# Optimization experiments

Hardware: AMD Instinct MI355X
Metric: run time of the kernel (lower is better)

Reference implementation:

```python
import jax, jax.numpy as jnp
import numpy as np

B, C, T, D = 4, 64, 256, 256   # batch, channel, time, in_feat
H, DK, OUT = 4, 64, 256        # heads, d_k, out_feat
MIN_VALUE = float(np.finfo(np.float32).min)


def _complex_linear(xr, xi, wr, wi, br, bi):
    # ComplexLinear: (fc_r(xr) - fc_i(xi), fc_r(xi) + fc_i(xr))
    out_r = (xr @ wr + br) - (xi @ wi + bi)
    out_i = (xi @ wr + br) + (xr @ wi + bi)
    return out_r, out_i


def setup_inputs() -> dict:
    key = jax.random.key(0)
    ks = jax.random.split(key, 23)
    s = 1.0 / np.sqrt(D)
    inp = {}
    names = ['q_r', 'q_i', 'k_r', 'k_i', 'v_r', 'v_i']
    for i, n in enumerate(names):
        inp[n] = jax.random.normal(ks[i], (B, C, T, D), dtype=jnp.float32)
    inp['mask'] = jnp.ones((B, 1, C), dtype=jnp.int32)
    pi = 6
    for proj in ['q', 'k', 'v', 'o']:
        out_dim = OUT if proj == 'o' else D
        inp[f'w{proj}_r'] = jax.random.normal(ks[pi], (D, out_dim), dtype=jnp.float32) * s; pi += 1
        inp[f'w{proj}_i'] = jax.random.normal(ks[pi], (D, out_dim), dtype=jnp.float32) * s; pi += 1
        inp[f'b{proj}_r'] = jax.random.normal(ks[pi], (out_dim,), dtype=jnp.float32) * 0.01; pi += 1
        inp[f'b{proj}_i'] = jax.random.normal(ks[pi], (out_dim,), dtype=jnp.float32) * 0.01; pi += 1
    return inp


def _split_heads(x):
    # (B, C, T, D) -> (B, H, T, C, DK)  [view + transpose(1,3)]
    return x.reshape(B, C, T, H, DK).transpose(0, 3, 2, 1, 4)


def _attention(q_r, q_i, k_r, k_i, v_r, v_i, mask,
               wq_r, wq_i, bq_r, bq_i, wk_r, wk_i, bk_r, bk_i,
               wv_r, wv_i, bv_r, bv_i, wo_r, wo_i, bo_r, bo_i):
    qr, qi = _complex_linear(q_r, q_i, wq_r, wq_i, bq_r, bq_i)
    kr, ki = _complex_linear(k_r, k_i, wk_r, wk_i, bk_r, bk_i)
    vr, vi = _complex_linear(v_r, v_i, wv_r, wv_i, bv_r, bv_i)
    qr, qi, kr, ki, vr, vi = map(_split_heads, (qr, qi, kr, ki, vr, vi))

    # scores = conj(q) @ k^T  (conjugate_transpose_matmul_conjugate), scaled by 1/sqrt(d_k)
    scale = 1.0 / np.sqrt(DK)
    s_r = (jnp.einsum('bhtcd,bhted->bhtce', qr, kr)
           + jnp.einsum('bhtcd,bhted->bhtce', qi, ki)) * scale
    s_i = (jnp.einsum('bhtcd,bhted->bhtce', qr, ki)
           - jnp.einsum('bhtcd,bhted->bhtce', qi, kr)) * scale

    # amplitude softmax with masking (mask: (B,1,C) -> (B,1,1,1,C), eq(0))
    mask_b = (mask == 0)[:, None, None]  # (B,1,1,1,C)
    amp = jnp.sqrt(s_r * s_r + s_i * s_i)
    amp = jnp.where(mask_b, MIN_VALUE, amp)
    sc = jax.nn.softmax(amp, axis=-1) / amp
    a_r = jnp.where(mask_b, 0.0, sc * s_r)
    a_i = jnp.where(mask_b, 0.0, sc * s_i)

    # complex matmul attn @ v
    x_r = (jnp.einsum('bhtce,bhted->bhtcd', a_r, vr)
           - jnp.einsum('bhtce,bhted->bhtcd', a_i, vi))
    x_i = (jnp.einsum('bhtce,bhted->bhtcd', a_i, vr)
           + jnp.einsum('bhtce,bhted->bhtcd', a_r, vi))

    # (B,H,T,C,DK) -> (B,C,T,H*DK)
    x_r = x_r.transpose(0, 3, 2, 1, 4).reshape(B, C, T, H * DK)
    x_i = x_i.transpose(0, 3, 2, 1, 4).reshape(B, C, T, H * DK)
    return _complex_linear(x_r, x_i, wo_r, wo_i, bo_r, bo_i)


def reference(q_r, q_i, k_r, k_i, v_r, v_i, mask,
              wq_r, wq_i, bq_r, bq_i, wk_r, wk_i, bk_r, bk_i,
              wv_r, wv_i, bv_r, bv_i, wo_r, wo_i, bo_r, bo_i):
    return _attention(q_r, q_i, k_r, k_i, v_r, v_i, mask,
                      wq_r, wq_i, bq_r, bq_i, wk_r, wk_i, bk_r, bk_i,
                      wv_r, wv_i, bv_r, bv_i, wo_r, wo_i, bo_r, bo_i)
```

## Files before the change

kernel.cpp:

```cpp
#include <hip/hip_runtime.h>
#include <hip/hip_bf16.h>
#include <cstddef>

#define MIN_VALUE_F (-3.402823466e38f)


typedef __attribute__((ext_vector_type(8))) __bf16 bfrag;
typedef __attribute__((ext_vector_type(4))) float f32x4;

__device__ __forceinline__ float bf2f(unsigned int u) {
    union { unsigned int i; float f; } v; v.i = u << 16; return v.f;
}
__device__ __forceinline__ unsigned short f2bf(float f) {
    union { float f; unsigned int i; } v; v.f = f;
    return (unsigned short)((v.i + 0x7fffu + ((v.i >> 16) & 1u)) >> 16);
}
__device__ __forceinline__ unsigned int cvt2(float a, float b) {
    __hip_bfloat16 lo = __float2bfloat16(a);
    __hip_bfloat16 hi = __float2bfloat16(b);
    union { __hip_bfloat16 h[2]; unsigned int u; } x;
    x.h[0] = lo; x.h[1] = hi;
    return x.u;
}
__device__ __forceinline__ bfrag negf(bfrag v) {
    union { bfrag b; unsigned int u[4]; } x; x.b = v;
    #pragma unroll
    for (int i = 0; i < 4; ++i) x.u[i] ^= 0x80008000u;
    return x.b;
}

typedef __attribute__((address_space(3))) void lds_void_t;
typedef const __attribute__((address_space(1))) void gmem_void_t;
__device__ __forceinline__ void glds16(const void* g, void* l) {
    __builtin_amdgcn_global_load_lds((gmem_void_t*)g, (lds_void_t*)l, 16, 0, 0);
}

__device__ __forceinline__ bfrag rdfrag(const unsigned short* arr, int row, int slot) {
    const int s = slot ^ (row & 7);
    return *(const bfrag*)&arr[row * 64 + s * 8];
}

__global__ __launch_bounds__(256)
void wprep_kernel(const float* __restrict__ w0, const float* __restrict__ w1,
                  const float* __restrict__ w2, const float* __restrict__ w3,
                  const float* __restrict__ w4, const float* __restrict__ w5,
                  unsigned short* __restrict__ dst)
{
    const int my = blockIdx.y;
    const float* wsrc[6] = {w0, w1, w2, w3, w4, w5};
    const float* w = wsrc[my];
    const int cid = blockIdx.x * 256 + threadIdx.x;
    const int img = cid >> 10;
    const int nb = img >> 2, s = img & 3;
    const int u0 = (cid & 1023) << 3;
    const int n_loc = u0 >> 6;
    const int k_src = (u0 & 63) ^ ((n_loc & 7) << 3);
    const int n = nb * 128 + n_loc;
    const int kbase = s * 64 + k_src;
    unsigned int p[4];
    #pragma unroll
    for (int jj = 0; jj < 4; ++jj) {
        const float a = w[(size_t)(kbase + 2 * jj) * 256 + n];
        const float b = w[(size_t)(kbase + 2 * jj + 1) * 256 + n];
        p[jj] = cvt2(a, b);
    }
    uint4 q; q.x = p[0]; q.y = p[1]; q.z = p[2]; q.w = p[3];
    *(uint4*)&dst[(size_t)my * 65536 + img * 8192 + u0] = q;
}

__global__ __launch_bounds__(256, 2)
void proj_mfma(const float* __restrict__ xq_r, const float* __restrict__ xq_i,
               const float* __restrict__ xk_r, const float* __restrict__ xk_i,
               const float* __restrict__ xv_r, const float* __restrict__ xv_i,
               const unsigned short* __restrict__ wimg,
               const float* __restrict__ bq_r, const float* __restrict__ bq_i,
               const float* __restrict__ bk_r, const float* __restrict__ bk_i,
               const float* __restrict__ bv_r, const float* __restrict__ bv_i,
               unsigned short* __restrict__ ws_out)
{
    __shared__ __align__(16) unsigned short As_r[8192], As_i[8192], Ws_r[8192], Ws_i[8192];
    const int pz = blockIdx.z;
    const float *xr, *xi, *br_, *bi_;
    if (pz == 0)      { xr = xq_r; xi = xq_i; br_ = bq_r; bi_ = bq_i; }
    else if (pz == 1) { xr = xk_r; xi = xk_i; br_ = bk_r; bi_ = bk_i; }
    else              { xr = xv_r; xi = xv_i; br_ = bv_r; bi_ = bv_i; }
    const unsigned short* wr_img = wimg + (size_t)pz * 131072;
    const unsigned short* wi_img = wr_img + 65536;
    unsigned short* outr = ws_out + (size_t)pz * 2 * 16777216;
    unsigned short* outi = outr + 16777216;

    const int tid = threadIdx.x;
    const int lane = tid & 63, wv = tid >> 6;
    const int wm = (wv >> 1) * 64, wn = (wv & 1) * 64;
    const int m0 = blockIdx.x * 128;
    const int nb = blockIdx.y;
    const int sm = tid >> 3;
    const int sk = (tid & 7) << 3;
    f32x4 accR[4][4] = {}, accI[4][4] = {};

    for (int s = 0; s < 4; ++s) {
        const unsigned short* wrp = wr_img + (nb * 4 + s) * 8192;
        const unsigned short* wip = wi_img + (nb * 4 + s) * 8192;
        #pragma unroll
        for (int cc = 0; cc < 4; ++cc) {
            const int offs = wv * 2048 + cc * 512;
            glds16(wrp + offs + lane * 8, &Ws_r[offs]);
            glds16(wip + offs + lane * 8, &Ws_i[offs]);
        }
        #pragma unroll
        for (int it = 0; it < 4; ++it) {
            const int m = it * 32 + sm;
            const float* sr = xr + (size_t)(m0 + m) * 256 + s * 64 + sk;
            const float* si = xi + (size_t)(m0 + m) * 256 + s * 64 + sk;
            const float4 a0 = *(const float4*)sr;
            const float4 a1 = *(const float4*)(sr + 4);
            const float4 b0 = *(const float4*)si;
            const float4 b1 = *(const float4*)(si + 4);
            const int idx = (m * 64 + sk) ^ ((m & 7) << 3);
            uint4 pr, pi;
            pr.x = cvt2(a0.x, a0.y); pr.y = cvt2(a0.z, a0.w);
            pr.z = cvt2(a1.x, a1.y); pr.w = cvt2(a1.z, a1.w);
            pi.x = cvt2(b0.x, b0.y); pi.y = cvt2(b0.z, b0.w);
            pi.z = cvt2(b1.x, b1.y); pi.w = cvt2(b1.z, b1.w);
            *(uint4*)&As_r[idx] = pr;
            *(uint4*)&As_i[idx] = pi;
        }
        __syncthreads();
        #pragma unroll
        for (int ks = 0; ks < 2; ++ks) {
            const int kb = ks * 32 + ((lane >> 4) << 3);
            bfrag ar[4], ai[4], nai[4];
            #pragma unroll
            for (int mf = 0; mf < 4; ++mf) {
                const int m = wm + mf * 16 + (lane & 15);
                const int idx = (m * 64 + kb) ^ ((m & 7) << 3);
                ar[mf] = *(const bfrag*)&As_r[idx];
                ai[mf] = *(const bfrag*)&As_i[idx];
                nai[mf] = negf(ai[mf]);
            }
            #pragma unroll
            for (int nf = 0; nf < 4; ++nf) {
                const int n = wn + nf * 16 + (lane & 15);
                const int idx = (n * 64 + kb) ^ ((n & 7) << 3);
                const bfrag brf = *(const bfrag*)&Ws_r[idx];
                const bfrag bif = *(const bfrag*)&Ws_i[idx];
                #pragma unroll
                for (int mf = 0; mf < 4; ++mf) {
                    accR[mf][nf] = __builtin_amdgcn_mfma_f32_16x16x32_bf16(ar[mf], brf, accR[mf][nf], 0, 0, 0);
                    accR[mf][nf] = __builtin_amdgcn_mfma_f32_16x16x32_bf16(nai[mf], bif, accR[mf][nf], 0, 0, 0);
                    accI[mf][nf] = __builtin_amdgcn_mfma_f32_16x16x32_bf16(ai[mf], brf, accI[mf][nf], 0, 0, 0);
                    accI[mf][nf] = __builtin_amdgcn_mfma_f32_16x16x32_bf16(ar[mf], bif, accI[mf][nf], 0, 0, 0);
                }
            }
        }
        __syncthreads();
    }
    const int bc = m0 >> 8, b = bc >> 6, c = bc & 63, t0 = m0 & 255;
    const int colL = lane & 15, rowL = (lane >> 4) << 2;
    #pragma unroll
    for (int nf = 0; nf < 4; ++nf) {
        const int n_glob = nb * 128 + wn + nf * 16 + colL;
        const int h = n_glob >> 6, dk = n_glob & 63;
        const float vbr = br_[n_glob], vbi = bi_[n_glob];
        const float addR = vbr - vbi, addI = vbr + vbi;
        const size_t baseh = (((size_t)(b * 4 + h) * 256) * 64 + c) * 64 + dk;
        #pragma unroll
        for (int mf = 0; mf < 4; ++mf) {
            const int tb = t0 + wm + mf * 16 + rowL;
            #pragma unroll
            for (int r = 0; r < 4; ++r) {
                const size_t o = baseh + (size_t)(tb + r) * 4096;
                outr[o] = f2bf(accR[mf][nf][r] + addR);
                outi[o] = f2bf(accI[mf][nf][r] + addI);
            }
        }
    }
}

__global__ __launch_bounds__(256)
void attn_mfma(const unsigned short* __restrict__ Qg_r, const unsigned short* __restrict__ Qg_i,
               const unsigned short* __restrict__ Kg_r, const unsigned short* __restrict__ Kg_i,
               const unsigned short* __restrict__ Vg_r, const unsigned short* __restrict__ Vg_i,
               const int* __restrict__ mask,
               unsigned short* __restrict__ Xr, unsigned short* __restrict__ Xi)
{
    __shared__ __align__(16) unsigned short sQr[4096], sQi[4096];
    __shared__ __align__(16) unsigned short sKr[4096], sKi[4096];
    __shared__ __align__(16) unsigned short sVr[4608], sVi[4608];
    __shared__ int smask[64];

    const int bht = blockIdx.x;
    const int b = bht >> 10;
    const int h = (bht >> 8) & 3;
    const int t = bht & 255;
    const size_t base = (size_t)bht * 4096;
    const int tid = threadIdx.x;
    const int lane = tid & 63, wv = tid >> 6;
    const int l15 = lane & 15, hi = lane >> 4;

    const int ep = (lane & 31) * 2;
    const int dch = wv * 2 + (lane >> 5);
    const unsigned short* vr0p = Vg_r + base + (size_t)ep * 64 + dch * 8;
    const unsigned short* vi0p = Vg_i + base + (size_t)ep * 64 + dch * 8;
    const uint4 vr0 = *(const uint4*)vr0p;
    const uint4 vr1 = *(const uint4*)(vr0p + 64);
    const uint4 vi0 = *(const uint4*)vi0p;
    const uint4 vi1 = *(const uint4*)(vi0p + 64);

    #pragma unroll
    for (int i = 0; i < 2; ++i) {
        const int ch = wv * 128 + i * 64 + lane;
        const int r = ch >> 3, cg = ch & 7;
        const int so = r * 64 + ((cg ^ (r & 7)) << 3);
        const int dofs = (wv * 128 + i * 64) << 3;
        glds16(Qg_r + base + so, &sQr[dofs]);
        glds16(Qg_i + base + so, &sQi[dofs]);
        glds16(Kg_r + base + so, &sKr[dofs]);
        glds16(Kg_i + base + so, &sKi[dofs]);
    }
    if (tid < 64) smask[tid] = mask[b * 64 + tid];

    {
        union { uint4 v; unsigned short s[8]; } ar0, ar1, ai0, ai1;
        ar0.v = vr0; ar1.v = vr1; ai0.v = vi0; ai1.v = vi1;
        #pragma unroll
        for (int j = 0; j < 8; ++j) {
            const int d = dch * 8 + j;
            *(unsigned int*)&sVr[d * 72 + ep] = (unsigned)ar0.s[j] | ((unsigned)ar1.s[j] << 16);
            *(unsigned int*)&sVi[d * 72 + ep] = (unsigned)ai0.s[j] | ((unsigned)ai1.s[j] << 16);
        }
    }
    __syncthreads();

    const int cq = wv * 16 + l15;
    f32x4 aR[4] = {}, aI[4] = {};
    #pragma unroll
    for (int ks = 0; ks < 2; ++ks) {
        const int slot = ks * 4 + hi;
        const bfrag qr = rdfrag(sQr, cq, slot);
        const bfrag qi = rdfrag(sQi, cq, slot);
        const bfrag nqi = negf(qi);
        #pragma unroll
        for (int et = 0; et < 4; ++et) {
            const int re = et * 16 + l15;
            const bfrag kr = rdfrag(sKr, re, slot);
            const bfrag ki = rdfrag(sKi, re, slot);
            aR[et] = __builtin_amdgcn_mfma_f32_16x16x32_bf16(kr, qr, aR[et], 0, 0, 0);
            aR[et] = __builtin_amdgcn_mfma_f32_16x16x32_bf16(ki, qi, aR[et], 0, 0, 0);
            aI[et] = __builtin_amdgcn_mfma_f32_16x16x32_bf16(ki, qr, aI[et], 0, 0, 0);
            aI[et] = __builtin_amdgcn_mfma_f32_16x16x32_bf16(kr, nqi, aI[et], 0, 0, 0);
        }
    }
    __syncthreads();

    const float scale = 0.125f;
    float amp[4][4], ex[4][4];
    float mx = MIN_VALUE_F;
    #pragma unroll
    for (int et = 0; et < 4; ++et) {
        #pragma unroll
        for (int r = 0; r < 4; ++r) {
            const float sr = aR[et][r] * scale;
            const float si = aI[et][r] * scale;
            float a = sqrtf(fmaf(sr, sr, si * si));
            if (smask[et * 16 + hi * 4 + r] == 0) a = MIN_VALUE_F;
            amp[et][r] = a;
            mx = fmaxf(mx, a);
        }
    }
    mx = fmaxf(mx, __shfl_xor(mx, 16, 64));
    mx = fmaxf(mx, __shfl_xor(mx, 32, 64));
    float sm = 0.f;
    #pragma unroll
    for (int et = 0; et < 4; ++et) {
        #pragma unroll
        for (int r = 0; r < 4; ++r) {
            const float e_ = expf(amp[et][r] - mx);
            ex[et][r] = e_; sm += e_;
        }
    }
    sm += __shfl_xor(sm, 16, 64);
    sm += __shfl_xor(sm, 32, 64);

    #pragma unroll
    for (int et = 0; et < 4; ++et) {
        float pr[4], pi[4];
        #pragma unroll
        for (int r = 0; r < 4; ++r) {
            const float w = ex[et][r] * __builtin_amdgcn_rcpf(sm * amp[et][r]);
            pr[r] = w * (aR[et][r] * scale);
            pi[r] = w * (aI[et][r] * scale);
        }
        const int pidx = cq * 64 + ((et * 16 + hi * 4) ^ ((cq & 7) << 3));
        uint2 ur, ui;
        ur.x = cvt2(pr[0], pr[1]); ur.y = cvt2(pr[2], pr[3]);
        ui.x = cvt2(pi[0], pi[1]); ui.y = cvt2(pi[2], pi[3]);
        *(uint2*)&sQr[pidx] = ur;
        *(uint2*)&sQi[pidx] = ui;
    }
    __syncthreads();

    f32x4 xR4[4] = {}, xI4[4] = {};
    #pragma unroll
    for (int ks = 0; ks < 2; ++ks) {
        const int slot = ks * 4 + hi;
        const bfrag pr = rdfrag(sQr, cq, slot);
        const bfrag pi = rdfrag(sQi, cq, slot);
        const bfrag npi = negf(pi);
        #pragma unroll
        for (int dt = 0; dt < 4; ++dt) {
            const int rd = dt * 16 + l15;
            const bfrag vr = *(const bfrag*)&sVr[rd * 72 + ks * 32 + hi * 8];
            const bfrag vi = *(const bfrag*)&sVi[rd * 72 + ks * 32 + hi * 8];
            xR4[dt] = __builtin_amdgcn_mfma_f32_16x16x32_bf16(pr, vr, xR4[dt], 0, 0, 0);
            xR4[dt] = __builtin_amdgcn_mfma_f32_16x16x32_bf16(npi, vi, xR4[dt], 0, 0, 0);
            xI4[dt] = __builtin_amdgcn_mfma_f32_16x16x32_bf16(pi, vr, xI4[dt], 0, 0, 0);
            xI4[dt] = __builtin_amdgcn_mfma_f32_16x16x32_bf16(pr, vi, xI4[dt], 0, 0, 0);
        }
    }

    #pragma unroll
    for (int dt = 0; dt < 4; ++dt) {
        #pragma unroll
        for (int r = 0; r < 4; ++r) {
            const int c = wv * 16 + hi * 4 + r;
            const size_t o = (((size_t)(b * 64 + c) * 256) + t) * 256 + h * 64 + dt * 16 + l15;
            Xr[o] = f2bf(xR4[dt][r]);
            Xi[o] = f2bf(xI4[dt][r]);
        }
    }
}

__global__ __launch_bounds__(256, 2)
void oproj_mfma(const unsigned short* __restrict__ Xr_g, const unsigned short* __restrict__ Xi_g,
                const unsigned short* __restrict__ wimg,
                const float* __restrict__ bo_r, const float* __restrict__ bo_i,
                float* __restrict__ outr, float* __restrict__ outi)
{
    __shared__ __align__(16) unsigned short As_r[8192], As_i[8192], Ws_r[8192], Ws_i[8192];
    const int tid = threadIdx.x;
    const int lane = tid & 63, wv = tid >> 6;
    const int wm = (wv >> 1) * 64, wn = (wv & 1) * 64;
    const int m0 = blockIdx.x * 128;
    const int nb = blockIdx.y;
    f32x4 accR[4][4] = {}, accI[4][4] = {};

    for (int s = 0; s < 4; ++s) {
        const unsigned short* wrp = wimg + (nb * 4 + s) * 8192;
        const unsigned short* wip = wimg + 65536 + (nb * 4 + s) * 8192;
        #pragma unroll
        for (int cc = 0; cc < 4; ++cc) {
            const int offs = wv * 2048 + cc * 512;
            glds16(wrp + offs + lane * 8, &Ws_r[offs]);
            glds16(wip + offs + lane * 8, &Ws_i[offs]);
            const int p = (offs + lane * 8) << 1;
            const int m = p >> 7;
            const int kl = ((p & 127) ^ ((m & 7) << 4)) >> 1;
            const size_t so = (size_t)(m0 + m) * 256 + s * 64 + kl;
            glds16(Xr_g + so, &As_r[offs]);
            glds16(Xi_g + so, &As_i[offs]);
        }
        __syncthreads();
        #pragma unroll
        for (int ks = 0; ks < 2; ++ks) {
            const int kb = ks * 32 + ((lane >> 4) << 3);
            bfrag ar[4], ai[4], nai[4];
            #pragma unroll
            for (int mf = 0; mf < 4; ++mf) {
                const int m = wm + mf * 16 + (lane & 15);
                const int idx = (m * 64 + kb) ^ ((m & 7) << 3);
                ar[mf] = *(const bfrag*)&As_r[idx];
                ai[mf] = *(const bfrag*)&As_i[idx];
                nai[mf] = negf(ai[mf]);
            }
            #pragma unroll
            for (int nf = 0; nf < 4; ++nf) {
                const int n = wn + nf * 16 + (lane & 15);
                const int idx = (n * 64 + kb) ^ ((n & 7) << 3);
                const bfrag brf = *(const bfrag*)&Ws_r[idx];
                const bfrag bif = *(const bfrag*)&Ws_i[idx];
                #pragma unroll
                for (int mf = 0; mf < 4; ++mf) {
                    accR[mf][nf] = __builtin_amdgcn_mfma_f32_16x16x32_bf16(ar[mf], brf, accR[mf][nf], 0, 0, 0);
                    accR[mf][nf] = __builtin_amdgcn_mfma_f32_16x16x32_bf16(nai[mf], bif, accR[mf][nf], 0, 0, 0);
                    accI[mf][nf] = __builtin_amdgcn_mfma_f32_16x16x32_bf16(ai[mf], brf, accI[mf][nf], 0, 0, 0);
                    accI[mf][nf] = __builtin_amdgcn_mfma_f32_16x16x32_bf16(ar[mf], bif, accI[mf][nf], 0, 0, 0);
                }
            }
        }
        __syncthreads();
    }
    const int colL = lane & 15, rowL = (lane >> 4) << 2;
    #pragma unroll
    for (int nf = 0; nf < 4; ++nf) {
        const int n = nb * 128 + wn + nf * 16 + colL;
        const float vbr = bo_r[n], vbi = bo_i[n];
        const float addR = vbr - vbi, addI = vbr + vbi;
        #pragma unroll
        for (int mf = 0; mf < 4; ++mf) {
            const int mb = m0 + wm + mf * 16 + rowL;
            #pragma unroll
            for (int r = 0; r < 4; ++r) {
                const size_t o = (size_t)(mb + r) * 256 + n;
                outr[o] = accR[mf][nf][r] + addR;
                outi[o] = accI[mf][nf][r] + addI;
            }
        }
    }
}

extern "C" void kernel_launch(void* const* d_in, const int* in_sizes, int n_in,
                              void* d_out, int out_size, void* d_ws, size_t ws_size,
                              hipStream_t stream)
{
    (void)in_sizes; (void)n_in; (void)out_size; (void)ws_size;
    const float* q_r = (const float*)d_in[0];
    const float* q_i = (const float*)d_in[1];
    const float* k_r = (const float*)d_in[2];
    const float* k_i = (const float*)d_in[3];
    const float* v_r = (const float*)d_in[4];
    const float* v_i = (const float*)d_in[5];
    const int* mask = (const int*)d_in[6];
    const float* wq_r = (const float*)d_in[7];
    const float* wq_i = (const float*)d_in[8];
    const float* bq_r = (const float*)d_in[9];
    const float* bq_i = (const float*)d_in[10];
    const float* wk_r = (const float*)d_in[11];
    const float* wk_i = (const float*)d_in[12];
    const float* bk_r = (const float*)d_in[13];
    const float* bk_i = (const float*)d_in[14];
    const float* wv_r = (const float*)d_in[15];
    const float* wv_i = (const float*)d_in[16];
    const float* bv_r = (const float*)d_in[17];
    const float* bv_i = (const float*)d_in[18];
    const float* wo_r = (const float*)d_in[19];
    const float* wo_i = (const float*)d_in[20];
    const float* bo_r = (const float*)d_in[21];
    const float* bo_i = (const float*)d_in[22];

    const size_t TS = 16777216;
    unsigned short* ws = (unsigned short*)d_ws;
    unsigned short* Q = ws;
    unsigned short* Xr = ws + 6 * TS;
    unsigned short* Xi = ws + 7 * TS;
    unsigned short* wimg_qkv = ws + 6 * TS;
    unsigned short* wimg_o = ws;

    wprep_kernel<<<dim3(32, 6), 256, 0, stream>>>(wq_r, wq_i, wk_r, wk_i, wv_r, wv_i, wimg_qkv);
    proj_mfma<<<dim3(512, 2, 3), 256, 0, stream>>>(q_r, q_i, k_r, k_i, v_r, v_i, wimg_qkv,
                                                   bq_r, bq_i, bk_r, bk_i, bv_r, bv_i, ws);
    attn_mfma<<<dim3(4096), 256, 0, stream>>>(Q, Q + TS, Q + 2 * TS, Q + 3 * TS,
                                              Q + 4 * TS, Q + 5 * TS, mask, Xr, Xi);
    wprep_kernel<<<dim3(32, 2), 256, 0, stream>>>(wo_r, wo_i, wo_r, wo_r, wo_r, wo_r, wimg_o);
    oproj_mfma<<<dim3(512, 2), 256, 0, stream>>>(Xr, Xi, wimg_o, bo_r, bo_i,
                                                 (float*)d_out, (float*)d_out + TS);
}
```

Baseline: 342.5 us.

## Register-prefetch next K-step and use 8 waves in projection GEMMs

Both projection GEMM kernels move from 256 to 512 threads, giving each wave a 64x32 output tile instead of 64x64. Global loads for the next K-step are issued into registers before the current step's MFMAs and written to LDS afterwards, replacing direct-to-LDS loads with a software pipeline. The QKV projection also stages its bf16 outputs through shared memory so the scattered head-split stores become 16-byte vector writes. This targets global-load latency and uncoalesced output stores, at the cost of more registers per thread and extra barriers.

```diff
diff --git a/kernel.cpp b/kernel.cpp
--- a/kernel.cpp
+++ b/kernel.cpp
@@ -68,7 +68,7 @@
     *(uint4*)&dst[(size_t)my * 65536 + img * 8192 + u0] = q;
 }
 
-__global__ __launch_bounds__(256, 2)
+__global__ __launch_bounds__(512, 2)
 void proj_mfma(const float* __restrict__ xq_r, const float* __restrict__ xq_i,
                const float* __restrict__ xk_r, const float* __restrict__ xk_i,
                const float* __restrict__ xv_r, const float* __restrict__ xv_i,
@@ -78,7 +78,12 @@
                const float* __restrict__ bv_r, const float* __restrict__ bv_i,
                unsigned short* __restrict__ ws_out)
 {
-    __shared__ __align__(16) unsigned short As_r[8192], As_i[8192], Ws_r[8192], Ws_i[8192];
+    __shared__ __align__(16) unsigned short SH[32768];
+    unsigned short* As_r = SH;
+    unsigned short* As_i = SH + 8192;
+    unsigned short* Ws_r = SH + 16384;
+    unsigned short* Ws_i = SH + 24576;
+
     const int pz = blockIdx.z;
     const float *xr, *xi, *br_, *bi_;
     if (pz == 0)      { xr = xq_r; xi = xq_i; br_ = bq_r; bi_ = bq_i; }
@@ -91,57 +96,80 @@
 
     const int tid = threadIdx.x;
     const int lane = tid & 63, wv = tid >> 6;
-    const int wm = (wv >> 1) * 64, wn = (wv & 1) * 64;
+    const int l15 = lane & 15;
+    const int wm = (wv >> 2) * 64, wn = (wv & 3) * 32;
     const int m0 = blockIdx.x * 128;
     const int nb = blockIdx.y;
-    const int sm = tid >> 3;
-    const int sk = (tid & 7) << 3;
-    f32x4 accR[4][4] = {}, accI[4][4] = {};
-
+
+    const int srow = tid >> 2;
+    const int skq = (tid & 3) << 4;
+    const int swz = (srow & 7) << 3;
+    const int rowb = srow * 64;
+    const float* arp = xr + (size_t)(m0 + srow) * 256 + skq;
+    const float* aip = xi + (size_t)(m0 + srow) * 256 + skq;
+    const uint4* wr32 = (const uint4*)(wr_img + nb * 4 * 8192);
+    const uint4* wi32 = (const uint4*)(wi_img + nb * 4 * 8192);
+
+    f32x4 accR[4][2] = {}, accI[4][2] = {};
+    float4 ar4[4], ai4[4];
+    uint4 wbr0, wbr1, wbi0, wbi1;
+
+    auto load_step = [&](int s) {
+        const float* a = arp + s * 64;
+        const float* b = aip + s * 64;
+        #pragma unroll
+        for (int j = 0; j < 4; ++j) {
+            ar4[j] = ((const float4*)a)[j];
+            ai4[j] = ((const float4*)b)[j];
+        }
+        wbr0 = wr32[s * 1024 + tid];
+        wbr1 = wr32[s * 1024 + 512 + tid];
+        wbi0 = wi32[s * 1024 + tid];
+        wbi1 = wi32[s * 1024 + 512 + tid];
+    };
+    auto write_stage = [&]() {
+        uint4 p0, p1, q0, q1;
+        p0.x = cvt2(ar4[0].x, ar4[0].y); p0.y = cvt2(ar4[0].z, ar4[0].w);
+        p0.z = cvt2(ar4[1].x, ar4[1].y); p0.w = cvt2(ar4[1].z, ar4[1].w);
+        p1.x = cvt2(ar4[2].x, ar4[2].y); p1.y = cvt2(ar4[2].z, ar4[2].w);
+        p1.z = cvt2(ar4[3].x, ar4[3].y); p1.w = cvt2(ar4[3].z, ar4[3].w);
+        q0.x = cvt2(ai4[0].x, ai4[0].y); q0.y = cvt2(ai4[0].z, ai4[0].w);
+        q0.z = cvt2(ai4[1].x, ai4[1].y); q0.w = cvt2(ai4[1].z, ai4[1].w);
+        q1.x = cvt2(ai4[2].x, ai4[2].y); q1.y = cvt2(ai4[2].z, ai4[2].w);
+        q1.z = cvt2(ai4[3].x, ai4[3].y); q1.w = cvt2(ai4[3].z, ai4[3].w);
+        *(uint4*)&As_r[rowb + (skq ^ swz)] = p0;
+        *(uint4*)&As_r[rowb + ((skq + 8) ^ swz)] = p1;
+        *(uint4*)&As_i[rowb + (skq ^ swz)] = q0;
+        *(uint4*)&As_i[rowb + ((skq + 8) ^ swz)] = q1;
+        *(uint4*)&Ws_r[tid * 8] = wbr0;
+        *(uint4*)&Ws_r[4096 + tid * 8] = wbr1;
+        *(uint4*)&Ws_i[tid * 8] = wbi0;
+        *(uint4*)&Ws_i[4096 + tid * 8] = wbi1;
+    };
+
+    load_step(0);
+    write_stage();
+    __syncthreads();
+
+    #pragma unroll
     for (int s = 0; s < 4; ++s) {
-        const unsigned short* wrp = wr_img + (nb * 4 + s) * 8192;
-        const unsigned short* wip = wi_img + (nb * 4 + s) * 8192;
-        #pragma unroll
-        for (int cc = 0; cc < 4; ++cc) {
-            const int offs = wv * 2048 + cc * 512;
-            glds16(wrp + offs + lane * 8, &Ws_r[offs]);
-            glds16(wip + offs + lane * 8, &Ws_i[offs]);
-        }
-        #pragma unroll
-        for (int it = 0; it < 4; ++it) {
-            const int m = it * 32 + sm;
-            const float* sr = xr + (size_t)(m0 + m) * 256 + s * 64 + sk;
-            const float* si = xi + (size_t)(m0 + m) * 256 + s * 64 + sk;
-            const float4 a0 = *(const float4*)sr;
-            const float4 a1 = *(const float4*)(sr + 4);
-            const float4 b0 = *(const float4*)si;
-            const float4 b1 = *(const float4*)(si + 4);
-            const int idx = (m * 64 + sk) ^ ((m & 7) << 3);
-            uint4 pr, pi;
-            pr.x = cvt2(a0.x, a0.y); pr.y = cvt2(a0.z, a0.w);
-            pr.z = cvt2(a1.x, a1.y); pr.w = cvt2(a1.z, a1.w);
-            pi.x = cvt2(b0.x, b0.y); pi.y = cvt2(b0.z, b0.w);
-            pi.z = cvt2(b1.x, b1.y); pi.w = cvt2(b1.z, b1.w);
-            *(uint4*)&As_r[idx] = pr;
-            *(uint4*)&As_i[idx] = pi;
-        }
-        __syncthreads();
+        if (s < 3) load_step(s + 1);
         #pragma unroll
         for (int ks = 0; ks < 2; ++ks) {
             const int kb = ks * 32 + ((lane >> 4) << 3);
             bfrag ar[4], ai[4], nai[4];
             #pragma unroll
             for (int mf = 0; mf < 4; ++mf) {
-                const int m = wm + mf * 16 + (lane & 15);
-                const int idx = (m * 64 + kb) ^ ((m & 7) << 3);
+                const int m = wm + mf * 16 + l15;
+                const int idx = m * 64 + (kb ^ ((m & 7) << 3));
                 ar[mf] = *(const bfrag*)&As_r[idx];
                 ai[mf] = *(const bfrag*)&As_i[idx];
                 nai[mf] = negf(ai[mf]);
             }
             #pragma unroll
-            for (int nf = 0; nf < 4; ++nf) {
-                const int n = wn + nf * 16 + (lane & 15);
-                const int idx = (n * 64 + kb) ^ ((n & 7) << 3);
+            for (int nf = 0; nf < 2; ++nf) {
+                const int n = wn + nf * 16 + l15;
+                const int idx = n * 64 + (kb ^ ((n & 7) << 3));
                 const bfrag brf = *(const bfrag*)&Ws_r[idx];
                 const bfrag bif = *(const bfrag*)&Ws_i[idx];
                 #pragma unroll
@@ -154,26 +182,38 @@
             }
         }
         __syncthreads();
-    }
+        if (s < 3) { write_stage(); __syncthreads(); }
+    }
+
     const int bc = m0 >> 8, b = bc >> 6, c = bc & 63, t0 = m0 & 255;
-    const int colL = lane & 15, rowL = (lane >> 4) << 2;
-    #pragma unroll
-    for (int nf = 0; nf < 4; ++nf) {
-        const int n_glob = nb * 128 + wn + nf * 16 + colL;
-        const int h = n_glob >> 6, dk = n_glob & 63;
+    const int rowL = (lane >> 4) << 2;
+    #pragma unroll
+    for (int nf = 0; nf < 2; ++nf) {
+        const int n_loc = wn + nf * 16 + l15;
+        const int n_glob = nb * 128 + n_loc;
+        const int hs = n_loc >> 6, dk = n_loc & 63;
         const float vbr = br_[n_glob], vbi = bi_[n_glob];
         const float addR = vbr - vbi, addI = vbr + vbi;
-        const size_t baseh = (((size_t)(b * 4 + h) * 256) * 64 + c) * 64 + dk;
         #pragma unroll
         for (int mf = 0; mf < 4; ++mf) {
-            const int tb = t0 + wm + mf * 16 + rowL;
+            const int tr = wm + mf * 16 + rowL;
             #pragma unroll
             for (int r = 0; r < 4; ++r) {
-                const size_t o = baseh + (size_t)(tb + r) * 4096;
-                outr[o] = f2bf(accR[mf][nf][r] + addR);
-                outi[o] = f2bf(accI[mf][nf][r] + addI);
+                const int L = hs * 8192 + (tr + r) * 64 + dk;
+                SH[L] = f2bf(accR[mf][nf][r] + addR);
+                SH[16384 + L] = f2bf(accI[mf][nf][r] + addI);
             }
         }
+    }
+    __syncthreads();
+    const int h0 = nb * 2;
+    #pragma unroll
+    for (int p = 0; p < 4; ++p) {
+        const int L = p * 4096 + tid * 8;
+        const int hs2 = L >> 13, tr2 = (L >> 6) & 127, dk2 = L & 63;
+        const size_t g = (((size_t)(b * 4 + h0 + hs2) * 256 + (t0 + tr2)) * 64 + c) * 64 + dk2;
+        *(uint4*)&outr[g] = *(const uint4*)&SH[L];
+        *(uint4*)&outi[g] = *(const uint4*)&SH[16384 + L];
     }
 }
 
@@ -331,52 +371,81 @@
     }
 }
 
-__global__ __launch_bounds__(256, 2)
+__global__ __launch_bounds__(512, 2)
 void oproj_mfma(const unsigned short* __restrict__ Xr_g, const unsigned short* __restrict__ Xi_g,
                 const unsigned short* __restrict__ wimg,
                 const float* __restrict__ bo_r, const float* __restrict__ bo_i,
                 float* __restrict__ outr, float* __restrict__ outi)
 {
-    __shared__ __align__(16) unsigned short As_r[8192], As_i[8192], Ws_r[8192], Ws_i[8192];
+    __shared__ __align__(16) unsigned short SH[32768];
+    unsigned short* As_r = SH;
+    unsigned short* As_i = SH + 8192;
+    unsigned short* Ws_r = SH + 16384;
+    unsigned short* Ws_i = SH + 24576;
+
     const int tid = threadIdx.x;
     const int lane = tid & 63, wv = tid >> 6;
-    const int wm = (wv >> 1) * 64, wn = (wv & 1) * 64;
+    const int l15 = lane & 15;
+    const int wm = (wv >> 2) * 64, wn = (wv & 3) * 32;
     const int m0 = blockIdx.x * 128;
     const int nb = blockIdx.y;
-    f32x4 accR[4][4] = {}, accI[4][4] = {};
-
+
+    const int srow = tid >> 2;
+    const int skq = (tid & 3) << 4;
+    const int swz = (srow & 7) << 3;
+    const int rowb = srow * 64;
+    const unsigned short* xrp = Xr_g + (size_t)(m0 + srow) * 256 + skq;
+    const unsigned short* xip = Xi_g + (size_t)(m0 + srow) * 256 + skq;
+    const uint4* wr32 = (const uint4*)(wimg + nb * 4 * 8192);
+    const uint4* wi32 = (const uint4*)(wimg + 65536 + nb * 4 * 8192);
+
+    f32x4 accR[4][2] = {}, accI[4][2] = {};
+    uint4 xbr0, xbr1, xbi0, xbi1, wbr0, wbr1, wbi0, wbi1;
+
+    auto load_step = [&](int s) {
+        const uint4* a = (const uint4*)(xrp + s * 64);
+        const uint4* bpt = (const uint4*)(xip + s * 64);
+        xbr0 = a[0]; xbr1 = a[1];
+        xbi0 = bpt[0]; xbi1 = bpt[1];
+        wbr0 = wr32[s * 1024 + tid];
+        wbr1 = wr32[s * 1024 + 512 + tid];
+        wbi0 = wi32[s * 1024 + tid];
+        wbi1 = wi32[s * 1024 + 512 + tid];
+    };
+    auto write_stage = [&]() {
+        *(uint4*)&As_r[rowb + (skq ^ swz)] = xbr0;
+        *(uint4*)&As_r[rowb + ((skq + 8) ^ swz)] = xbr1;
+        *(uint4*)&As_i[rowb + (skq ^ swz)] = xbi0;
+        *(uint4*)&As_i[rowb + ((skq + 8) ^ swz)] = xbi1;
+        *(uint4*)&Ws_r[tid * 8] = wbr0;
+        *(uint4*)&Ws_r[4096 + tid * 8] = wbr1;
+        *(uint4*)&Ws_i[tid * 8] = wbi0;
+        *(uint4*)&Ws_i[4096 + tid * 8] = wbi1;
+    };
+
+    load_step(0);
+    write_stage();
+    __syncthreads();
+
+    #pragma unroll
     for (int s = 0; s < 4; ++s) {
-        const unsigned short* wrp = wimg + (nb * 4 + s) * 8192;
-        const unsigned short* wip = wimg + 65536 + (nb * 4 + s) * 8192;
-        #pragma unroll
-        for (int cc = 0; cc < 4; ++cc) {
-            const int offs = wv * 2048 + cc * 512;
-            glds16(wrp + offs + lane * 8, &Ws_r[offs]);
-            glds16(wip + offs + lane * 8, &Ws_i[offs]);
-            const int p = (offs + lane * 8) << 1;
-            const int m = p >> 7;
-            const int kl = ((p & 127) ^ ((m & 7) << 4)) >> 1;
-            const size_t so = (size_t)(m0 + m) * 256 + s * 64 + kl;
-            glds16(Xr_g + so, &As_r[offs]);
-            glds16(Xi_g + so, &As_i[offs]);
-        }
-        __syncthreads();
+        if (s < 3) load_step(s + 1);
         #pragma unroll
         for (int ks = 0; ks < 2; ++ks) {
             const int kb = ks * 32 + ((lane >> 4) << 3);
             bfrag ar[4], ai[4], nai[4];
             #pragma unroll
             for (int mf = 0; mf < 4; ++mf) {
-                const int m = wm + mf * 16 + (lane & 15);
-                const int idx = (m * 64 + kb) ^ ((m & 7) << 3);
+                const int m = wm + mf * 16 + l15;
+                const int idx = m * 64 + (kb ^ ((m & 7) << 3));
                 ar[mf] = *(const bfrag*)&As_r[idx];
                 ai[mf] = *(const bfrag*)&As_i[idx];
                 nai[mf] = negf(ai[mf]);
             }
             #pragma unroll
-            for (int nf = 0; nf < 4; ++nf) {
-                const int n = wn + nf * 16 + (lane & 15);
-                const int idx = (n * 64 + kb) ^ ((n & 7) << 3);
+            for (int nf = 0; nf < 2; ++nf) {
+                const int n = wn + nf * 16 + l15;
+                const int idx = n * 64 + (kb ^ ((n & 7) << 3));
                 const bfrag brf = *(const bfrag*)&Ws_r[idx];
                 const bfrag bif = *(const bfrag*)&Ws_i[idx];
                 #pragma unroll
@@ -389,11 +458,13 @@
             }
         }
         __syncthreads();
-    }
-    const int colL = lane & 15, rowL = (lane >> 4) << 2;
-    #pragma unroll
-    for (int nf = 0; nf < 4; ++nf) {
-        const int n = nb * 128 + wn + nf * 16 + colL;
+        if (s < 3) { write_stage(); __syncthreads(); }
+    }
+
+    const int rowL = (lane >> 4) << 2;
+    #pragma unroll
+    for (int nf = 0; nf < 2; ++nf) {
+        const int n = nb * 128 + wn + nf * 16 + l15;
         const float vbr = bo_r[n], vbi = bo_i[n];
         const float addR = vbr - vbi, addI = vbr + vbi;
         #pragma unroll
@@ -447,11 +518,11 @@
     unsigned short* wimg_o = ws;
 
     wprep_kernel<<<dim3(32, 6), 256, 0, stream>>>(wq_r, wq_i, wk_r, wk_i, wv_r, wv_i, wimg_qkv);
-    proj_mfma<<<dim3(512, 2, 3), 256, 0, stream>>>(q_r, q_i, k_r, k_i, v_r, v_i, wimg_qkv,
+    proj_mfma<<<dim3(512, 2, 3), 512, 0, stream>>>(q_r, q_i, k_r, k_i, v_r, v_i, wimg_qkv,
                                                    bq_r, bq_i, bk_r, bk_i, bv_r, bv_i, ws);
     attn_mfma<<<dim3(4096), 256, 0, stream>>>(Q, Q + TS, Q + 2 * TS, Q + 3 * TS,
                                               Q + 4 * TS, Q + 5 * TS, mask, Xr, Xi);
     wprep_kernel<<<dim3(32, 2), 256, 0, stream>>>(wo_r, wo_i, wo_r, wo_r, wo_r, wo_r, wimg_o);
-    oproj_mfma<<<dim3(512, 2), 256, 0, stream>>>(Xr, Xi, wimg_o, bo_r, bo_i,
+    oproj_mfma<<<dim3(512, 2), 512, 0, stream>>>(Xr, Xi, wimg_o, bo_r, bo_i,
                                                  (float*)d_out, (float*)d_out + TS);
 }
```

Measured after the change: 350.5 us. 2.4% more time.

## Double-buffer projection GEMMs with 32x32 MFMA and fragment-ordered weight images

Applied to the files above, without the earlier changes.

Rewrites the QKV and output projection GEMMs to use 32x32x16 bf16 MFMA with a register-prefetched, double-buffered LDS pipeline over eight K=32 stages. The weight-prep kernel now emits weights pre-arranged in MFMA fragment order so they can be copied straight into LDS. Block indices are remapped so blocks are spread across XCDs, and the QKV epilogue stages results in LDS so the head-split layout is written with 16-byte stores. The cost is more launches, a different LDS layout, and more registers per thread.

```diff
diff --git a/kernel.cpp b/kernel.cpp
--- a/kernel.cpp
+++ b/kernel.cpp
@@ -7,6 +7,7 @@
 
 typedef __attribute__((ext_vector_type(8))) __bf16 bfrag;
 typedef __attribute__((ext_vector_type(4))) float f32x4;
+typedef __attribute__((ext_vector_type(16))) float f32x16;
 
 __device__ __forceinline__ float bf2f(unsigned int u) {
     union { unsigned int i; float f; } v; v.i = u << 16; return v.f;
@@ -41,32 +42,57 @@
 }
 
 __global__ __launch_bounds__(256)
-void wprep_kernel(const float* __restrict__ w0, const float* __restrict__ w1,
-                  const float* __restrict__ w2, const float* __restrict__ w3,
-                  const float* __restrict__ w4, const float* __restrict__ w5,
+void wprep_kernel(const float* __restrict__ wr, const float* __restrict__ wi,
                   unsigned short* __restrict__ dst)
 {
-    const int my = blockIdx.y;
-    const float* wsrc[6] = {w0, w1, w2, w3, w4, w5};
-    const float* w = wsrc[my];
     const int cid = blockIdx.x * 256 + threadIdx.x;
-    const int img = cid >> 10;
-    const int nb = img >> 2, s = img & 3;
-    const int u0 = (cid & 1023) << 3;
-    const int n_loc = u0 >> 6;
-    const int k_src = (u0 & 63) ^ ((n_loc & 7) << 3);
-    const int n = nb * 128 + n_loc;
-    const int kbase = s * 64 + k_src;
+    const int lane = cid & 63;
+    const int h  = (cid >> 6) & 1;
+    const int g  = (cid >> 7) & 3;
+    const int s  = (cid >> 9) & 7;
+    const int ri = (cid >> 12) & 1;
+    const int nt = cid >> 13;
+    const float* w = ri ? wi : wr;
+    const int col = nt * 128 + g * 32 + (lane & 31);
+    const int kb = s * 32 + h * 16 + (lane >> 5) * 8;
     unsigned int p[4];
     #pragma unroll
     for (int jj = 0; jj < 4; ++jj) {
-        const float a = w[(size_t)(kbase + 2 * jj) * 256 + n];
-        const float b = w[(size_t)(kbase + 2 * jj + 1) * 256 + n];
+        const float a = w[(size_t)(kb + 2 * jj) * 256 + col];
+        const float b = w[(size_t)(kb + 2 * jj + 1) * 256 + col];
         p[jj] = cvt2(a, b);
     }
     uint4 q; q.x = p[0]; q.y = p[1]; q.z = p[2]; q.w = p[3];
-    *(uint4*)&dst[(size_t)my * 65536 + img * 8192 + u0] = q;
-}
+    *(uint4*)&dst[(size_t)cid * 8] = q;
+}
+
+#define P_LOADA(s) { \
+    const size_t oA_ = (size_t)(m0 + rA) * 256 + (s) * 32 + aq * 8; \
+    const size_t oB_ = oA_ + (size_t)64 * 256; \
+    fra0 = *(const float4*)(xr + oA_);  fra1 = *(const float4*)(xr + oA_ + 4); \
+    frb0 = *(const float4*)(xr + oB_);  frb1 = *(const float4*)(xr + oB_ + 4); \
+    fia0 = *(const float4*)(xi + oA_);  fia1 = *(const float4*)(xi + oA_ + 4); \
+    fib0 = *(const float4*)(xi + oB_);  fib1 = *(const float4*)(xi + oB_ + 4); }
+
+#define P_LOADW(s) { \
+    wbr0 = wru[(s) * 512 + tid];  wbr1 = wru[(s) * 512 + 256 + tid]; \
+    wbi0 = wiu[(s) * 512 + tid];  wbi1 = wiu[(s) * 512 + 256 + tid]; }
+
+#define PK4(d_, v0_, v1_) { \
+    d_.x = cvt2(v0_.x, v0_.y); d_.y = cvt2(v0_.z, v0_.w); \
+    d_.z = cvt2(v1_.x, v1_.y); d_.w = cvt2(v1_.z, v1_.w); }
+
+#define P_WRITE(buf) { \
+    unsigned short* B_ = SH + (buf) * 16384; \
+    uint4 t_; \
+    PK4(t_, fra0, fra1); *(uint4*)&B_[idxA] = t_; \
+    PK4(t_, frb0, frb1); *(uint4*)&B_[idxA + 2048] = t_; \
+    PK4(t_, fia0, fia1); *(uint4*)&B_[4096 + idxA] = t_; \
+    PK4(t_, fib0, fib1); *(uint4*)&B_[4096 + idxA + 2048] = t_; \
+    *(uint4*)&B_[8192 + tid * 8] = wbr0; \
+    *(uint4*)&B_[8192 + (256 + tid) * 8] = wbr1; \
+    *(uint4*)&B_[12288 + tid * 8] = wbi0; \
+    *(uint4*)&B_[12288 + (256 + tid) * 8] = wbi1; }
 
 __global__ __launch_bounds__(256, 2)
 void proj_mfma(const float* __restrict__ xq_r, const float* __restrict__ xq_i,
@@ -78,102 +104,106 @@
                const float* __restrict__ bv_r, const float* __restrict__ bv_i,
                unsigned short* __restrict__ ws_out)
 {
-    __shared__ __align__(16) unsigned short As_r[8192], As_i[8192], Ws_r[8192], Ws_i[8192];
-    const int pz = blockIdx.z;
+    __shared__ __align__(16) unsigned short SH[32768];
+
+    const int bid = blockIdx.x;
+    const int work = (bid & 7) * 384 + (bid >> 3);
+    const int ny = work & 1;
+    const int m0 = ((work >> 1) & 511) * 128;
+    const int pz = work >> 10;
+
     const float *xr, *xi, *br_, *bi_;
     if (pz == 0)      { xr = xq_r; xi = xq_i; br_ = bq_r; bi_ = bq_i; }
     else if (pz == 1) { xr = xk_r; xi = xk_i; br_ = bk_r; bi_ = bk_i; }
     else              { xr = xv_r; xi = xv_i; br_ = bv_r; bi_ = bv_i; }
-    const unsigned short* wr_img = wimg + (size_t)pz * 131072;
-    const unsigned short* wi_img = wr_img + 65536;
     unsigned short* outr = ws_out + (size_t)pz * 2 * 16777216;
     unsigned short* outi = outr + 16777216;
 
     const int tid = threadIdx.x;
     const int lane = tid & 63, wv = tid >> 6;
+    const int l31 = lane & 31, khl = lane >> 5;
     const int wm = (wv >> 1) * 64, wn = (wv & 1) * 64;
-    const int m0 = blockIdx.x * 128;
-    const int nb = blockIdx.y;
-    const int sm = tid >> 3;
-    const int sk = (tid & 7) << 3;
-    f32x4 accR[4][4] = {}, accI[4][4] = {};
-
-    for (int s = 0; s < 4; ++s) {
-        const unsigned short* wrp = wr_img + (nb * 4 + s) * 8192;
-        const unsigned short* wip = wi_img + (nb * 4 + s) * 8192;
-        #pragma unroll
-        for (int cc = 0; cc < 4; ++cc) {
-            const int offs = wv * 2048 + cc * 512;
-            glds16(wrp + offs + lane * 8, &Ws_r[offs]);
-            glds16(wip + offs + lane * 8, &Ws_i[offs]);
-        }
-        #pragma unroll
-        for (int it = 0; it < 4; ++it) {
-            const int m = it * 32 + sm;
-            const float* sr = xr + (size_t)(m0 + m) * 256 + s * 64 + sk;
-            const float* si = xi + (size_t)(m0 + m) * 256 + s * 64 + sk;
-            const float4 a0 = *(const float4*)sr;
-            const float4 a1 = *(const float4*)(sr + 4);
-            const float4 b0 = *(const float4*)si;
-            const float4 b1 = *(const float4*)(si + 4);
-            const int idx = (m * 64 + sk) ^ ((m & 7) << 3);
-            uint4 pr, pi;
-            pr.x = cvt2(a0.x, a0.y); pr.y = cvt2(a0.z, a0.w);
-            pr.z = cvt2(a1.x, a1.y); pr.w = cvt2(a1.z, a1.w);
-            pi.x = cvt2(b0.x, b0.y); pi.y = cvt2(b0.z, b0.w);
-            pi.z = cvt2(b1.x, b1.y); pi.w = cvt2(b1.z, b1.w);
-            *(uint4*)&As_r[idx] = pr;
-            *(uint4*)&As_i[idx] = pi;
-        }
+    const int wmg = wm >> 5, wng = wn >> 5;
+
+    const unsigned short* wbase = wimg + (size_t)pz * 131072 + ny * 65536;
+    const uint4* wru = (const uint4*)wbase;
+    const uint4* wiu = (const uint4*)(wbase + 32768);
+
+    const int rA = tid >> 2;
+    const int aq = tid & 3;
+    const int idxA = (((rA >> 5) * 2 + (aq >> 1)) * 64 + (rA & 31) + (aq & 1) * 32) * 8;
+
+    float4 fra0, fra1, frb0, frb1, fia0, fia1, fib0, fib1;
+    uint4 wbr0, wbr1, wbi0, wbi1;
+
+    f32x16 accR[2][2] = {}, accI[2][2] = {};
+
+    P_LOADA(0); P_LOADW(0);
+    P_WRITE(0);
+    __syncthreads();
+
+    #pragma unroll
+    for (int s = 0; s < 8; ++s) {
+        if (s < 7) { P_LOADA(s + 1); P_LOADW(s + 1); }
+        const unsigned short* Ab = SH + (s & 1) * 16384;
+        #pragma unroll
+        for (int h = 0; h < 2; ++h) {
+            bfrag ar[2], ai[2], nai[2], br[2], bi[2];
+            #pragma unroll
+            for (int mf = 0; mf < 2; ++mf) {
+                const int off = (((wmg + mf) * 2 + h) * 64 + lane) * 8;
+                ar[mf] = *(const bfrag*)&Ab[off];
+                ai[mf] = *(const bfrag*)&Ab[4096 + off];
+                nai[mf] = negf(ai[mf]);
+            }
+            #pragma unroll
+            for (int nf = 0; nf < 2; ++nf) {
+                const int off = (((wng + nf) * 2 + h) * 64 + lane) * 8;
+                br[nf] = *(const bfrag*)&Ab[8192 + off];
+                bi[nf] = *(const bfrag*)&Ab[12288 + off];
+            }
+            #pragma unroll
+            for (int mf = 0; mf < 2; ++mf) {
+                #pragma unroll
+                for (int nf = 0; nf < 2; ++nf) {
+                    accR[mf][nf] = __builtin_amdgcn_mfma_f32_32x32x16_bf16(ar[mf], br[nf], accR[mf][nf], 0, 0, 0);
+                    accR[mf][nf] = __builtin_amdgcn_mfma_f32_32x32x16_bf16(nai[mf], bi[nf], accR[mf][nf], 0, 0, 0);
+                    accI[mf][nf] = __builtin_amdgcn_mfma_f32_32x32x16_bf16(ai[mf], br[nf], accI[mf][nf], 0, 0, 0);
+                    accI[mf][nf] = __builtin_amdgcn_mfma_f32_32x32x16_bf16(ar[mf], bi[nf], accI[mf][nf], 0, 0, 0);
+                }
+            }
+        }
+        if (s < 7) P_WRITE((s + 1) & 1);
         __syncthreads();
-        #pragma unroll
-        for (int ks = 0; ks < 2; ++ks) {
-            const int kb = ks * 32 + ((lane >> 4) << 3);
-            bfrag ar[4], ai[4], nai[4];
-            #pragma unroll
-            for (int mf = 0; mf < 4; ++mf) {
-                const int m = wm + mf * 16 + (lane & 15);
-                const int idx = (m * 64 + kb) ^ ((m & 7) << 3);
-                ar[mf] = *(const bfrag*)&As_r[idx];
-                ai[mf] = *(const bfrag*)&As_i[idx];
-                nai[mf] = negf(ai[mf]);
-            }
-            #pragma unroll
-            for (int nf = 0; nf < 4; ++nf) {
-                const int n = wn + nf * 16 + (lane & 15);
-                const int idx = (n * 64 + kb) ^ ((n & 7) << 3);
-                const bfrag brf = *(const bfrag*)&Ws_r[idx];
-                const bfrag bif = *(const bfrag*)&Ws_i[idx];
-                #pragma unroll
-                for (int mf = 0; mf < 4; ++mf) {
-                    accR[mf][nf] = __builtin_amdgcn_mfma_f32_16x16x32_bf16(ar[mf], brf, accR[mf][nf], 0, 0, 0);
-                    accR[mf][nf] = __builtin_amdgcn_mfma_f32_16x16x32_bf16(nai[mf], bif, accR[mf][nf], 0, 0, 0);
-                    accI[mf][nf] = __builtin_amdgcn_mfma_f32_16x16x32_bf16(ai[mf], brf, accI[mf][nf], 0, 0, 0);
-                    accI[mf][nf] = __builtin_amdgcn_mfma_f32_16x16x32_bf16(ar[mf], bif, accI[mf][nf], 0, 0, 0);
-                }
-            }
-        }
-        __syncthreads();
-    }
+    }
+
     const int bc = m0 >> 8, b = bc >> 6, c = bc & 63, t0 = m0 & 255;
-    const int colL = lane & 15, rowL = (lane >> 4) << 2;
-    #pragma unroll
-    for (int nf = 0; nf < 4; ++nf) {
-        const int n_glob = nb * 128 + wn + nf * 16 + colL;
-        const int h = n_glob >> 6, dk = n_glob & 63;
+    #pragma unroll
+    for (int nf = 0; nf < 2; ++nf) {
+        const int n_loc = wn + nf * 32 + l31;
+        const int n_glob = ny * 128 + n_loc;
         const float vbr = br_[n_glob], vbi = bi_[n_glob];
         const float addR = vbr - vbi, addI = vbr + vbi;
-        const size_t baseh = (((size_t)(b * 4 + h) * 256) * 64 + c) * 64 + dk;
-        #pragma unroll
-        for (int mf = 0; mf < 4; ++mf) {
-            const int tb = t0 + wm + mf * 16 + rowL;
-            #pragma unroll
-            for (int r = 0; r < 4; ++r) {
-                const size_t o = baseh + (size_t)(tb + r) * 4096;
-                outr[o] = f2bf(accR[mf][nf][r] + addR);
-                outi[o] = f2bf(accI[mf][nf][r] + addI);
-            }
-        }
+        #pragma unroll
+        for (int mf = 0; mf < 2; ++mf) {
+            #pragma unroll
+            for (int reg = 0; reg < 16; ++reg) {
+                const int m_loc = wm + mf * 32 + (reg & 3) + 8 * (reg >> 2) + 4 * khl;
+                SH[m_loc * 128 + n_loc] = f2bf(accR[mf][nf][reg] + addR);
+                SH[16384 + m_loc * 128 + n_loc] = f2bf(accI[mf][nf][reg] + addI);
+            }
+        }
+    }
+    __syncthreads();
+    const int h0 = ny * 2;
+    #pragma unroll
+    for (int p = 0; p < 8; ++p) {
+        const int L = p * 2048 + tid * 8;
+        const int mloc = L >> 7, nloc = L & 127;
+        const int hh = nloc >> 6, dk = nloc & 63;
+        const size_t g = (((size_t)(b * 4 + h0 + hh) * 256 + (t0 + mloc)) * 64 + c) * 64 + dk;
+        *(uint4*)&outr[g] = *(const uint4*)&SH[L];
+        *(uint4*)&outi[g] = *(const uint4*)&SH[16384 + L];
     }
 }
 
@@ -331,79 +361,109 @@
     }
 }
 
+#define O_LOADX(s) { \
+    const size_t oA_ = (size_t)(m0 + rA) * 256 + (s) * 32 + aq * 8; \
+    const size_t oB_ = oA_ + (size_t)64 * 256; \
+    xra = *(const uint4*)(Xr_g + oA_);  xrb = *(const uint4*)(Xr_g + oB_); \
+    xia = *(const uint4*)(Xi_g + oA_);  xib = *(const uint4*)(Xi_g + oB_); }
+
+#define O_LOADW(s) { \
+    wbr0 = wru[(s) * 512 + tid];  wbr1 = wru[(s) * 512 + 256 + tid]; \
+    wbi0 = wiu[(s) * 512 + tid];  wbi1 = wiu[(s) * 512 + 256 + tid]; }
+
+#define O_WRITE(buf) { \
+    unsigned short* B_ = SH + (buf) * 16384; \
+    *(uint4*)&B_[idxA] = xra; \
+    *(uint4*)&B_[idxA + 2048] = xrb; \
+    *(uint4*)&B_[4096 + idxA] = xia; \
+    *(uint4*)&B_[4096 + idxA + 2048] = xib; \
+    *(uint4*)&B_[8192 + tid * 8] = wbr0; \
+    *(uint4*)&B_[8192 + (256 + tid) * 8] = wbr1; \
+    *(uint4*)&B_[12288 + tid * 8] = wbi0; \
+    *(uint4*)&B_[12288 + (256 + tid) * 8] = wbi1; }
+
 __global__ __launch_bounds__(256, 2)
 void oproj_mfma(const unsigned short* __restrict__ Xr_g, const unsigned short* __restrict__ Xi_g,
                 const unsigned short* __restrict__ wimg,
                 const float* __restrict__ bo_r, const float* __restrict__ bo_i,
                 float* __restrict__ outr, float* __restrict__ outi)
 {
-    __shared__ __align__(16) unsigned short As_r[8192], As_i[8192], Ws_r[8192], Ws_i[8192];
+    __shared__ __align__(16) unsigned short SH[32768];
+
+    const int bid = blockIdx.x;
+    const int work = (bid & 7) * 128 + (bid >> 3);
+    const int ny = work & 1;
+    const int m0 = (work >> 1) * 128;
+
     const int tid = threadIdx.x;
     const int lane = tid & 63, wv = tid >> 6;
+    const int l31 = lane & 31, khl = lane >> 5;
     const int wm = (wv >> 1) * 64, wn = (wv & 1) * 64;
-    const int m0 = blockIdx.x * 128;
-    const int nb = blockIdx.y;
-    f32x4 accR[4][4] = {}, accI[4][4] = {};
-
-    for (int s = 0; s < 4; ++s) {
-        const unsigned short* wrp = wimg + (nb * 4 + s) * 8192;
-        const unsigned short* wip = wimg + 65536 + (nb * 4 + s) * 8192;
-        #pragma unroll
-        for (int cc = 0; cc < 4; ++cc) {
-            const int offs = wv * 2048 + cc * 512;
-            glds16(wrp + offs + lane * 8, &Ws_r[offs]);
-            glds16(wip + offs + lane * 8, &Ws_i[offs]);
-            const int p = (offs + lane * 8) << 1;
-            const int m = p >> 7;
-            const int kl = ((p & 127) ^ ((m & 7) << 4)) >> 1;
-            const size_t so = (size_t)(m0 + m) * 256 + s * 64 + kl;
-            glds16(Xr_g + so, &As_r[offs]);
-            glds16(Xi_g + so, &As_i[offs]);
-        }
+    const int wmg = wm >> 5, wng = wn >> 5;
+
+    const unsigned short* wbase = wimg + ny * 65536;
+    const uint4* wru = (const uint4*)wbase;
+    const uint4* wiu = (const uint4*)(wbase + 32768);
+
+    const int rA = tid >> 2;
+    const int aq = tid & 3;
+    const int idxA = (((rA >> 5) * 2 + (aq >> 1)) * 64 + (rA & 31) + (aq & 1) * 32) * 8;
+
+    uint4 xra, xrb, xia, xib, wbr0, wbr1, wbi0, wbi1;
+
+    f32x16 accR[2][2] = {}, accI[2][2] = {};
+
+    O_LOADX(0); O_LOADW(0);
+    O_WRITE(0);
+    __syncthreads();
+
+    #pragma unroll
+    for (int s = 0; s < 8; ++s) {
+        if (s < 7) { O_LOADX(s + 1); O_LOADW(s + 1); }
+        const unsigned short* Ab = SH + (s & 1) * 16384;
+        #pragma unroll
+        for (int h = 0; h < 2; ++h) {
+            bfrag ar[2], ai[2], nai[2], br[2], bi[2];
+            #pragma unroll
+            for (int mf = 0; mf < 2; ++mf) {
+                const int off = (((wmg + mf) * 2 + h) * 64 + lane) * 8;
+                ar[mf] = *(const bfrag*)&Ab[off];
+                ai[mf] = *(const bfrag*)&Ab[4096 + off];
+                nai[mf] = negf(ai[mf]);
+            }
+            #pragma unroll
+            for (int nf = 0; nf < 2; ++nf) {
+                const int off = (((wng + nf) * 2 + h) * 64 + lane) * 8;
+                br[nf] = *(const bfrag*)&Ab[8192 + off];
+                bi[nf] = *(const bfrag*)&Ab[12288 + off];
+            }
+            #pragma unroll
+            for (int mf = 0; mf < 2; ++mf) {
+                #pragma unroll
+                for (int nf = 0; nf < 2; ++nf) {
+                    accR[mf][nf] = __builtin_amdgcn_mfma_f32_32x32x16_bf16(ar[mf], br[nf], accR[mf][nf], 0, 0, 0);
+                    accR[mf][nf] = __builtin_amdgcn_mfma_f32_32x32x16_bf16(nai[mf], bi[nf], accR[mf][nf], 0, 0, 0);
+                    accI[mf][nf] = __builtin_amdgcn_mfma_f32_32x32x16_bf16(ai[mf], br[nf], accI[mf][nf], 0, 0, 0);
+                    accI[mf][nf] = __builtin_amdgcn_mfma_f32_32x32x16_bf16(ar[mf], bi[nf], accI[mf][nf], 0, 0, 0);
+                }
+            }
+        }
+        if (s < 7) O_WRITE((s + 1) & 1);
         __syncthreads();
-        #pragma unroll
-        for (int ks = 0; ks < 2; ++ks) {
-            const int kb = ks * 32 + ((lane >> 4) << 3);
-            bfrag ar[4], ai[4], nai[4];
-            #pragma unroll
-            for (int mf = 0; mf < 4; ++mf) {
-                const int m = wm + mf * 16 + (lane & 15);
-                const int idx = (m * 64 + kb) ^ ((m & 7) << 3);
-                ar[mf] = *(const bfrag*)&As_r[idx];
-                ai[mf] = *(const bfrag*)&As_i[idx];
-                nai[mf] = negf(ai[mf]);
-            }
-            #pragma unroll
-            for (int nf = 0; nf < 4; ++nf) {
-                const int n = wn + nf * 16 + (lane & 15);
-                const int idx = (n * 64 + kb) ^ ((n & 7) << 3);
-                const bfrag brf = *(const bfrag*)&Ws_r[idx];
-                const bfrag bif = *(const bfrag*)&Ws_i[idx];
-                #pragma unroll
-                for (int mf = 0; mf < 4; ++mf) {
-                    accR[mf][nf] = __builtin_amdgcn_mfma_f32_16x16x32_bf16(ar[mf], brf, accR[mf][nf], 0, 0, 0);
-                    accR[mf][nf] = __builtin_amdgcn_mfma_f32_16x16x32_bf16(nai[mf], bif, accR[mf][nf], 0, 0, 0);
-                    accI[mf][nf] = __builtin_amdgcn_mfma_f32_16x16x32_bf16(ai[mf], brf, accI[mf][nf], 0, 0, 0);
-                    accI[mf][nf] = __builtin_amdgcn_mfma_f32_16x16x32_bf16(ar[mf], bif, accI[mf][nf], 0, 0, 0);
-                }
-            }
-        }
-        __syncthreads();
-    }
-    const int colL = lane & 15, rowL = (lane >> 4) << 2;
-    #pragma unroll
-    for (int nf = 0; nf < 4; ++nf) {
-        const int n = nb * 128 + wn + nf * 16 + colL;
+    }
+
+    #pragma unroll
+    for (int nf = 0; nf < 2; ++nf) {
+        const int n = ny * 128 + wn + nf * 32 + l31;
         const float vbr = bo_r[n], vbi = bo_i[n];
         const float addR = vbr - vbi, addI = vbr + vbi;
         #pragma unroll
-        for (int mf = 0; mf < 4; ++mf) {
-            const int mb = m0 + wm + mf * 16 + rowL;
-            #pragma unroll
-            for (int r = 0; r < 4; ++r) {
-                const size_t o = (size_t)(mb + r) * 256 + n;
-                outr[o] = accR[mf][nf][r] + addR;
-                outi[o] = accI[mf][nf][r] + addI;
+        for (int mf = 0; mf < 2; ++mf) {
+            #pragma unroll
+            for (int reg = 0; reg < 16; ++reg) {
+                const int m = m0 + wm + mf * 32 + (reg & 3) + 8 * (reg >> 2) + 4 * khl;
+                outr[(size_t)m * 256 + n] = accR[mf][nf][reg] + addR;
+                outi[(size_t)m * 256 + n] = accI[mf][nf][reg] + addI;
             }
         }
     }
@@ -446,12 +506,14 @@
     unsigned short* wimg_qkv = ws + 6 * TS;
     unsigned short* wimg_o = ws;
 
-    wprep_kernel<<<dim3(32, 6), 256, 0, stream>>>(wq_r, wq_i, wk_r, wk_i, wv_r, wv_i, wimg_qkv);
-    proj_mfma<<<dim3(512, 2, 3), 256, 0, stream>>>(q_r, q_i, k_r, k_i, v_r, v_i, wimg_qkv,
-                                                   bq_r, bq_i, bk_r, bk_i, bv_r, bv_i, ws);
+    wprep_kernel<<<dim3(64), 256, 0, stream>>>(wq_r, wq_i, wimg_qkv);
+    wprep_kernel<<<dim3(64), 256, 0, stream>>>(wk_r, wk_i, wimg_qkv + 131072);
+    wprep_kernel<<<dim3(64), 256, 0, stream>>>(wv_r, wv_i, wimg_qkv + 262144);
+    proj_mfma<<<dim3(3072), 256, 0, stream>>>(q_r, q_i, k_r, k_i, v_r, v_i, wimg_qkv,
+                                              bq_r, bq_i, bk_r, bk_i, bv_r, bv_i, ws);
     attn_mfma<<<dim3(4096), 256, 0, stream>>>(Q, Q + TS, Q + 2 * TS, Q + 3 * TS,
                                               Q + 4 * TS, Q + 5 * TS, mask, Xr, Xi);
-    wprep_kernel<<<dim3(32, 2), 256, 0, stream>>>(wo_r, wo_i, wo_r, wo_r, wo_r, wo_r, wimg_o);
-    oproj_mfma<<<dim3(512, 2), 256, 0, stream>>>(Xr, Xi, wimg_o, bo_r, bo_i,
-                                                 (float*)d_out, (float*)d_out + TS);
-}
+    wprep_kernel<<<dim3(64), 256, 0, stream>>>(wo_r, wo_i, wimg_o);
+    oproj_mfma<<<dim3(1024), 256, 0, stream>>>(Xr, Xi, wimg_o, bo_r, bo_i,
+                                               (float*)d_out, (float*)d_out + TS);
+}
```

Result: faster. 334.1 us (-2.4%).
